# Performance work log

Hardware: AMD Instinct MI355X
Metric: run time of the kernel (lower is better)

The kernel has to match this reference:

```python
import jax, jax.numpy as jnp
import numpy as np

RADIUS = 1.0
N_NORM = 1  # default n_norm in the torch module


def setup_inputs() -> dict:
    key = jax.random.key(0)
    k1, k2, k3 = jax.random.split(key, 3)
    batch, n, c_in, c_out = 8, 2048, 64, 64
    features = jax.random.normal(k1, (batch, n, c_in), dtype=jnp.float32)
    geometry = jax.random.normal(k2, (batch, n, 3), dtype=jnp.float32)
    # learned per-edge kernel weight: K(diff)[o,i] = sum_x diff[x] * Wk[x,o,i]
    Wk = jax.random.normal(k3, (3, c_out, c_in), dtype=jnp.float32) * 0.1
    return {"features": features, "geometry": geometry, "Wk": Wk}


def reference(features, geometry, Wk):
    # diff[z,a,b,:] = geometry[z,b] - geometry[z,a]   (rb - ra in the torch code)
    diff = geometry[:, None, :, :] - geometry[:, :, None, :]  # [z, a, b, 3]
    norm = jnp.sqrt(jnp.sum(diff * diff, axis=-1))            # [z, a, b]
    # Dense masked formulation: padding every point's neighbor list to k = n
    # with rel_mask zeros is mathematically identical to the torch variable-k
    # padding (masked entries contribute nothing to the einsum reduce).
    rel_mask = (norm < RADIUS).astype(features.dtype)         # [z, a, b]
    # Fused reduce. Original: einsum('zab,zabij,zabj->zai', mask, K(diff), feat[nei])
    # with K(diff)[z,a,b,i,j] = einsum('zabx,xij->zabij', diff, Wk). We contract
    # over b first to avoid materializing the [z,a,b,i,j] kernel tensor.
    s = jnp.einsum('zab,zabx,zbj->zaxj', rel_mask, diff, features)  # [z, a, 3, c_in]
    out = jnp.einsum('zaxj,xij->zai', s, Wk) / jnp.sqrt(jnp.asarray(N_NORM, features.dtype))
    return out
```

## Files before the change

### kernel.cpp

```cpp
#include <hip/hip_runtime.h>
#include <stdint.h>

#define NPTS 2048

#define BP_OFF    0ULL
#define BP_BYTES  (8ULL * 16 * 64 * 1024)
#define W2F_OFF   (BP_OFF + BP_BYTES)
#define W2F_BYTES (24ULL * 1024)
#define WXF_OFF   (W2F_OFF + W2F_BYTES)
#define WXF_BYTES (24ULL * 1024)
#define MW_OFF    (WXF_OFF + WXF_BYTES)
#define MW_BYTES  (8ULL * 32 * 64 * 256)

typedef __attribute__((ext_vector_type(8))) short bf16x8;
typedef __attribute__((ext_vector_type(4))) float f32x4;
typedef __attribute__((ext_vector_type(4))) unsigned int u32x4;

__device__ __forceinline__ unsigned f2bf(float f) {
  union { float f; unsigned u; } v; v.f = f;
  return (v.u + 0x7FFFu + ((v.u >> 16) & 1u)) >> 16;
}

__device__ __forceinline__ bf16x8 unpack_mask(unsigned mq) {
  const unsigned dep0 = ((mq & 15u) * 0x204081u) & 0x01010101u;
  const unsigned dep1 = (((mq >> 4) & 15u) * 0x204081u) & 0x01010101u;
  u32x4 aw;
  aw[0] = __builtin_amdgcn_perm(dep0, 0u, 0x0C050C04u) * 0x3F80u;
  aw[1] = __builtin_amdgcn_perm(dep0, 0u, 0x0C070C06u) * 0x3F80u;
  aw[2] = __builtin_amdgcn_perm(dep1, 0u, 0x0C050C04u) * 0x3F80u;
  aw[3] = __builtin_amdgcn_perm(dep1, 0u, 0x0C070C06u) * 0x3F80u;
  union { u32x4 u; bf16x8 h; } cv; cv.u = aw;
  return cv.h;
}

__global__ __launch_bounds__(256, 2) void k1_prep(const float* __restrict__ feat,
                                                  const float* __restrict__ geom,
                                                  const float* __restrict__ Wk,
                                                  unsigned char* __restrict__ ws) {
  const int blk = blockIdx.x, t = threadIdx.x;
  if (blk < 512) {
    const int z = blk >> 6, s = blk & 63;
    __shared__ float FT[64][37];
    __shared__ float g[96];
    __shared__ float gxp[2048], gyp[2048], gzp[2048];
    const float* fz = feat + ((size_t)z * NPTS + s * 32) * 64;
    const float* gz = geom + (size_t)z * NPTS * 3;
    {
      const int row = t >> 3, j0 = (t & 7) << 3;
      const float4 v0 = *(const float4*)&fz[row * 64 + j0];
      const float4 v1 = *(const float4*)&fz[row * 64 + j0 + 4];
      FT[j0 + 0][row] = v0.x; FT[j0 + 1][row] = v0.y;
      FT[j0 + 2][row] = v0.z; FT[j0 + 3][row] = v0.w;
      FT[j0 + 4][row] = v1.x; FT[j0 + 5][row] = v1.y;
      FT[j0 + 6][row] = v1.z; FT[j0 + 7][row] = v1.w;
    }
    if (t < 96) g[t] = gz[s * 96 + t];
    {
      float v[24];
#pragma unroll
      for (int i = 0; i < 6; ++i) *(float4*)&v[i * 4] = *(const float4*)&gz[t * 24 + i * 4];
#pragma unroll
      for (int i = 0; i < 8; ++i) {
        const int pp = i * 256 + t;
        gxp[pp] = v[i * 3 + 0]; gyp[pp] = v[i * 3 + 1]; gzp[pp] = v[i * 3 + 2];
      }
    }
    __syncthreads();

    {
      const int w = t >> 6, L = t & 63;
      const int nn = L >> 2, k0 = (L & 3) * 8;
      const int j = w * 16 + nn;
      float f[8];
#pragma unroll
      for (int i = 0; i < 8; ++i) f[i] = FT[j][k0 + i];
      float gx[3][8];
#pragma unroll
      for (int x = 0; x < 3; ++x)
#pragma unroll
        for (int i = 0; i < 8; ++i) gx[x][i] = g[(k0 + i) * 3 + x];
      unsigned char* base = ws + BP_OFF + (size_t)z * 1048576 + (size_t)w * 65536 +
                            (size_t)s * 1024 + L * 16;
#pragma unroll
      for (int it = 0; it < 4; ++it) {
        u32x4 pv;
#pragma unroll
        for (int p = 0; p < 4; ++p) {
          float f0 = f[2 * p], f1 = f[2 * p + 1];
          if (it < 3) { f0 *= gx[it][2 * p]; f1 *= gx[it][2 * p + 1]; }
          pv[p] = f2bf(f0) | (f2bf(f1) << 16);
        }
        *(u32x4*)(base + (size_t)it * 4 * 65536) = pv;
      }
    }

    {
      float ax[8], ay[8], az[8];
#pragma unroll
      for (int i = 0; i < 8; ++i) {
        const int pp = i * 256 + t;
        ax[i] = gxp[pp]; ay[i] = gyp[pp]; az[i] = gzp[pp];
      }
      unsigned bits[8] = {0, 0, 0, 0, 0, 0, 0, 0};
      for (int j = 0; j < 32; ++j) {
        const float bx = g[j * 3 + 0], by = g[j * 3 + 1], bz = g[j * 3 + 2];
#pragma unroll
        for (int i = 0; i < 8; ++i) {
          const float d0 = bx - ax[i], d1 = by - ay[i], d2 = bz - az[i];
          const float n2 = fmaf(d2, d2, fmaf(d1, d1, d0 * d0));
          bits[i] |= (n2 < 1.0f ? 1u : 0u) << j;
        }
      }
      unsigned int* mw = (unsigned int*)(ws + MW_OFF);
#pragma unroll
      for (int i = 0; i < 8; ++i) {
        const int r = t * 8 + i;
        mw[(((size_t)z * 32 + (r >> 6)) * 64 + s) * 64 + (r & 15) * 4 + ((r >> 4) & 3)] = bits[i];
      }
    }
  } else if (blk == 512) {
    for (int e = t; e < 1536; e += 256) {
      const int frag = e >> 6, lp = e & 63, nn = lp >> 2, qd = lp & 3;
      const int kb = frag >> 2, cb = frag & 3;
      u32x4 pv;
#pragma unroll
      for (int p = 0; p < 4; ++p) {
        const int k0 = kb * 32 + qd * 8 + 2 * p;
        const float v0 = Wk[(k0 >> 6) * 4096 + (cb * 16 + nn) * 64 + (k0 & 63)];
        const float v1 = Wk[((k0 + 1) >> 6) * 4096 + (cb * 16 + nn) * 64 + ((k0 + 1) & 63)];
        pv[p] = f2bf(v0) | (f2bf(v1) << 16);
      }
      *(u32x4*)(ws + W2F_OFF + (size_t)frag * 1024 + lp * 16) = pv;
    }
  } else {
    for (int e = t; e < 1536; e += 256) {
      const int frag = e >> 6, lp = e & 63, nn = lp >> 2, qd = lp & 3;
      const int kb = frag / 12, cb = frag % 12, xi = cb * 16 + nn;
      u32x4 pv;
#pragma unroll
      for (int p = 0; p < 4; ++p) {
        const int k0 = kb * 32 + qd * 8 + 2 * p;
        const float v0 = Wk[(xi >> 6) * 4096 + (xi & 63) * 64 + k0];
        const float v1 = Wk[(xi >> 6) * 4096 + (xi & 63) * 64 + k0 + 1];
        pv[p] = f2bf(v0) | (f2bf(v1) << 16);
      }
      *(u32x4*)(ws + WXF_OFF + (size_t)frag * 1024 + lp * 16) = pv;
    }
  }
}

__global__ __launch_bounds__(256, 2) void k2_gemm(const float* __restrict__ geom,
                                                  const unsigned char* __restrict__ ws,
                                                  float* __restrict__ out) {
  __shared__ __align__(16) unsigned short Ct[64 * 128];

  const int t = threadIdx.x, lane = t & 63, w = t >> 6;
  const int quad = (lane >> 4) & 3, n = lane & 15;
  const int bx = blockIdx.x;
  const int z = bx & 7, at = (bx >> 3) & 31, ch = bx >> 8;
  const int a0 = at * 64;
  const int fragoff = n * 64 + quad * 16;
  const int qsh = quad * 8;

  const unsigned char* bpz = ws + BP_OFF + (size_t)z * 1048576 +
                             (size_t)(ch * 8 + 2 * w) * 65536;
  const unsigned char* mwz = ws + MW_OFF + ((size_t)z * 32 + at) * 16384;

  f32x4 acc[4][2];
#pragma unroll
  for (int rg = 0; rg < 4; ++rg)
#pragma unroll
    for (int cb = 0; cb < 2; ++cb)
#pragma unroll
      for (int r = 0; r < 4; ++r) acc[rg][cb][r] = 0.f;

  bf16x8 Bf[2][2];
  u32x4 Mf[2];
#pragma unroll
  for (int sl = 0; sl < 2; ++sl) {
#pragma unroll
    for (int cb = 0; cb < 2; ++cb)
      Bf[sl][cb] = *(const bf16x8*)(bpz + (size_t)cb * 65536 + (size_t)sl * 1024 + fragoff);
    Mf[sl] = *(const u32x4*)(mwz + sl * 256 + n * 16);
  }

#define KSTEP(S, SL)                                                           \
  {                                                                            \
    const u32x4 mw = Mf[SL];                                                   \
    _Pragma("unroll") for (int rg = 0; rg < 4; ++rg) {                         \
      const bf16x8 Af = unpack_mask((mw[rg] >> qsh) & 0xFFu);                  \
      _Pragma("unroll") for (int cb = 0; cb < 2; ++cb)                         \
        acc[rg][cb] = __builtin_amdgcn_mfma_f32_16x16x32_bf16(                 \
            Af, Bf[SL][cb], acc[rg][cb], 0, 0, 0);                             \
    }                                                                          \
    const int sp = (S) + 2 > 63 ? 63 : (S) + 2;                                \
    Mf[SL] = *(const u32x4*)(mwz + sp * 256 + n * 16);                         \
    _Pragma("unroll") for (int cb = 0; cb < 2; ++cb)                           \
      Bf[SL][cb] = *(const bf16x8*)(bpz + (size_t)cb * 65536 +                 \
                                    (size_t)sp * 1024 + fragoff);              \
  }

  for (int s2 = 0; s2 < 64; s2 += 2) {
    KSTEP(s2, 0)
    KSTEP(s2 + 1, 1)
  }
#undef KSTEP

#pragma unroll
  for (int rg = 0; rg < 4; ++rg)
#pragma unroll
    for (int cb = 0; cb < 2; ++cb)
#pragma unroll
      for (int r = 0; r < 4; ++r) {
        const int row = rg * 16 + quad * 4 + r;
        const int col = w * 32 + cb * 16 + n;
        Ct[row * 128 + ((((col >> 3) ^ (row & 15)) & 15) << 3) + (col & 7)] =
            (unsigned short)f2bf(acc[rg][cb][r]);
      }
  __syncthreads();

  const int lm = 16 * w + n;
  bf16x8 Across[4];
#pragma unroll
  for (int kbl = 0; kbl < 4; ++kbl) {
    const int chunk = ((kbl * 4 + quad) ^ (lm & 15)) & 15;
    Across[kbl] = *(const bf16x8*)&Ct[lm * 128 + (chunk << 3)];
  }

  const unsigned char* w2f = ws + W2F_OFF;
  const unsigned char* wxf = ws + WXF_OFF;

  if (ch == 0) {
    f32x4 mn[4];
#pragma unroll
    for (int i = 0; i < 4; ++i)
#pragma unroll
      for (int r = 0; r < 4; ++r) mn[i][r] = 0.f;
#pragma unroll
    for (int kbl = 0; kbl < 4; ++kbl)
#pragma unroll
      for (int cb = 0; cb < 4; ++cb) {
        const bf16x8 Bfr = *(const bf16x8*)(w2f + (size_t)(kbl * 4 + cb) * 1024 + fragoff);
        mn[cb] = __builtin_amdgcn_mfma_f32_16x16x32_bf16(Across[kbl], Bfr, mn[cb], 0, 0, 0);
      }
#pragma unroll
    for (int r = 0; r < 4; ++r) {
      const int af = a0 + 16 * w + quad * 4 + r;
#pragma unroll
      for (int cb = 0; cb < 4; ++cb)
        atomicAdd(&out[((size_t)z * NPTS + af) * 64 + cb * 16 + n], mn[cb][r]);
    }
  } else {
    f32x4 mn[4], V[12];
#pragma unroll
    for (int i = 0; i < 4; ++i)
#pragma unroll
      for (int r = 0; r < 4; ++r) mn[i][r] = 0.f;
#pragma unroll
    for (int i = 0; i < 12; ++i)
#pragma unroll
      for (int r = 0; r < 4; ++r) V[i][r] = 0.f;
#pragma unroll
    for (int kbl = 0; kbl < 2; ++kbl)
#pragma unroll
      for (int cb = 0; cb < 4; ++cb) {
        const bf16x8 Bfr = *(const bf16x8*)(w2f + (size_t)((4 + kbl) * 4 + cb) * 1024 + fragoff);
        mn[cb] = __builtin_amdgcn_mfma_f32_16x16x32_bf16(Across[kbl], Bfr, mn[cb], 0, 0, 0);
      }
#pragma unroll
    for (int kbl = 0; kbl < 2; ++kbl)
#pragma unroll
      for (int cb = 0; cb < 12; ++cb) {
        const bf16x8 Bfr = *(const bf16x8*)(wxf + (size_t)(kbl * 12 + cb) * 1024 + fragoff);
        V[cb] = __builtin_amdgcn_mfma_f32_16x16x32_bf16(Across[2 + kbl], Bfr, V[cb], 0, 0, 0);
      }
#pragma unroll
    for (int r = 0; r < 4; ++r) {
      const int af = a0 + 16 * w + quad * 4 + r;
      const float g0 = geom[((size_t)z * NPTS + af) * 3 + 0];
      const float g1 = geom[((size_t)z * NPTS + af) * 3 + 1];
      const float g2 = geom[((size_t)z * NPTS + af) * 3 + 2];
#pragma unroll
      for (int cb = 0; cb < 4; ++cb) {
        const float v = mn[cb][r] - g0 * V[cb][r] - g1 * V[cb + 4][r] - g2 * V[cb + 8][r];
        atomicAdd(&out[((size_t)z * NPTS + af) * 64 + cb * 16 + n], v);
      }
    }
  }
}

extern "C" void kernel_launch(void* const* d_in, const int* in_sizes, int n_in,
                              void* d_out, int out_size, void* d_ws, size_t ws_size,
                              hipStream_t stream) {
  const float* feat = (const float*)d_in[0];
  const float* geom = (const float*)d_in[1];
  const float* Wk   = (const float*)d_in[2];
  float* out = (float*)d_out;
  unsigned char* ws = (unsigned char*)d_ws;

  hipMemsetAsync(out, 0, (size_t)out_size * sizeof(float), stream);
  k1_prep<<<dim3(514), 256, 0, stream>>>(feat, geom, Wk, ws);
  k2_gemm<<<dim3(512), 256, 0, stream>>>(geom, ws, out);
}
```

Measured before the change: 108.6 us.

## Merge K-split blocks into 512-thread blocks, drop atomics and memset

Each 64-point tile, previously split across two 256-thread blocks by channel half, is now handled by one 512-thread block whose eight waves cover all 256 columns. Partial results are staged in fp32 shared memory, and four waves run the full second-stage GEMM with plain stores. This removes the output memset and the atomicAdd traffic, and the prefetch depth in the main loop grows from 2 to 4 steps. In exchange the grid is halved to 256 blocks, which may leave CUs idle, register pressure rises from the deeper prefetch, and the epilogue uses only half the waves.

```diff
diff --git a/kernel.cpp b/kernel.cpp
--- a/kernel.cpp
+++ b/kernel.cpp
@@ -19,6 +19,15 @@
 __device__ __forceinline__ unsigned f2bf(float f) {
   union { float f; unsigned u; } v; v.f = f;
   return (v.u + 0x7FFFu + ((v.u >> 16) & 1u)) >> 16;
+}
+
+__device__ __forceinline__ bf16x8 pack8(const float4 a, const float4 b) {
+  u32x4 r;
+  r[0] = f2bf(a.x) | (f2bf(a.y) << 16);
+  r[1] = f2bf(a.z) | (f2bf(a.w) << 16);
+  r[2] = f2bf(b.x) | (f2bf(b.y) << 16);
+  r[3] = f2bf(b.z) | (f2bf(b.w) << 16);
+  union { u32x4 u; bf16x8 h; } c; c.u = r; return c.h;
 }
 
 __device__ __forceinline__ bf16x8 unpack_mask(unsigned mq) {
@@ -149,21 +158,19 @@
   }
 }
 
-__global__ __launch_bounds__(256, 2) void k2_gemm(const float* __restrict__ geom,
+__global__ __launch_bounds__(512, 2) void k2_gemm(const float* __restrict__ geom,
                                                   const unsigned char* __restrict__ ws,
                                                   float* __restrict__ out) {
-  __shared__ __align__(16) unsigned short Ct[64 * 128];
+  __shared__ __align__(16) float Ct[64 * 256];
 
   const int t = threadIdx.x, lane = t & 63, w = t >> 6;
   const int quad = (lane >> 4) & 3, n = lane & 15;
   const int bx = blockIdx.x;
-  const int z = bx & 7, at = (bx >> 3) & 31, ch = bx >> 8;
-  const int a0 = at * 64;
+  const int z = bx & 7, at = bx >> 3, a0 = at * 64;
   const int fragoff = n * 64 + quad * 16;
   const int qsh = quad * 8;
 
-  const unsigned char* bpz = ws + BP_OFF + (size_t)z * 1048576 +
-                             (size_t)(ch * 8 + 2 * w) * 65536;
+  const unsigned char* bpz = ws + BP_OFF + (size_t)z * 1048576 + (size_t)(2 * w) * 65536;
   const unsigned char* mwz = ws + MW_OFF + ((size_t)z * 32 + at) * 16384;
 
   f32x4 acc[4][2];
@@ -174,10 +181,10 @@
 #pragma unroll
       for (int r = 0; r < 4; ++r) acc[rg][cb][r] = 0.f;
 
-  bf16x8 Bf[2][2];
-  u32x4 Mf[2];
-#pragma unroll
-  for (int sl = 0; sl < 2; ++sl) {
+  bf16x8 Bf[4][2];
+  u32x4 Mf[4];
+#pragma unroll
+  for (int sl = 0; sl < 4; ++sl) {
 #pragma unroll
     for (int cb = 0; cb < 2; ++cb)
       Bf[sl][cb] = *(const bf16x8*)(bpz + (size_t)cb * 65536 + (size_t)sl * 1024 + fragoff);
@@ -193,16 +200,15 @@
         acc[rg][cb] = __builtin_amdgcn_mfma_f32_16x16x32_bf16(                 \
             Af, Bf[SL][cb], acc[rg][cb], 0, 0, 0);                             \
     }                                                                          \
-    const int sp = (S) + 2 > 63 ? 63 : (S) + 2;                                \
+    const int sp = (S) + 4 > 63 ? 63 : (S) + 4;                                \
     Mf[SL] = *(const u32x4*)(mwz + sp * 256 + n * 16);                         \
     _Pragma("unroll") for (int cb = 0; cb < 2; ++cb)                           \
       Bf[SL][cb] = *(const bf16x8*)(bpz + (size_t)cb * 65536 +                 \
                                     (size_t)sp * 1024 + fragoff);              \
   }
 
-  for (int s2 = 0; s2 < 64; s2 += 2) {
-    KSTEP(s2, 0)
-    KSTEP(s2 + 1, 1)
+  for (int s4 = 0; s4 < 64; s4 += 4) {
+    KSTEP(s4 + 0, 0) KSTEP(s4 + 1, 1) KSTEP(s4 + 2, 2) KSTEP(s4 + 3, 3)
   }
 #undef KSTEP
 
@@ -213,67 +219,50 @@
 #pragma unroll
       for (int r = 0; r < 4; ++r) {
         const int row = rg * 16 + quad * 4 + r;
-        const int col = w * 32 + cb * 16 + n;
-        Ct[row * 128 + ((((col >> 3) ^ (row & 15)) & 15) << 3) + (col & 7)] =
-            (unsigned short)f2bf(acc[rg][cb][r]);
+        const int col = 32 * w + cb * 16 + n;
+        Ct[row * 256 + (((col >> 2) ^ row) << 2) + (col & 3)] = acc[rg][cb][r];
       }
   __syncthreads();
 
-  const int lm = 16 * w + n;
-  bf16x8 Across[4];
-#pragma unroll
-  for (int kbl = 0; kbl < 4; ++kbl) {
-    const int chunk = ((kbl * 4 + quad) ^ (lm & 15)) & 15;
-    Across[kbl] = *(const bf16x8*)&Ct[lm * 128 + (chunk << 3)];
-  }
-
-  const unsigned char* w2f = ws + W2F_OFF;
-  const unsigned char* wxf = ws + WXF_OFF;
-
-  if (ch == 0) {
-    f32x4 mn[4];
+  if (w < 4) {
+    const int lm = 16 * w + n;
+    bf16x8 Across[8];
+#pragma unroll
+    for (int kb = 0; kb < 8; ++kb) {
+      const int c0 = (kb * 8 + quad * 2) ^ lm;
+      const int c1 = (kb * 8 + quad * 2 + 1) ^ lm;
+      const float4 f0 = *(const float4*)&Ct[lm * 256 + c0 * 4];
+      const float4 f1 = *(const float4*)&Ct[lm * 256 + c1 * 4];
+      Across[kb] = pack8(f0, f1);
+    }
+
+    f32x4 mn[4], V[12];
 #pragma unroll
     for (int i = 0; i < 4; ++i)
 #pragma unroll
       for (int r = 0; r < 4; ++r) mn[i][r] = 0.f;
 #pragma unroll
-    for (int kbl = 0; kbl < 4; ++kbl)
+    for (int i = 0; i < 12; ++i)
+#pragma unroll
+      for (int r = 0; r < 4; ++r) V[i][r] = 0.f;
+
+    const unsigned char* w2f = ws + W2F_OFF;
+    const unsigned char* wxf = ws + WXF_OFF;
+#pragma unroll
+    for (int kb = 0; kb < 6; ++kb)
 #pragma unroll
       for (int cb = 0; cb < 4; ++cb) {
-        const bf16x8 Bfr = *(const bf16x8*)(w2f + (size_t)(kbl * 4 + cb) * 1024 + fragoff);
-        mn[cb] = __builtin_amdgcn_mfma_f32_16x16x32_bf16(Across[kbl], Bfr, mn[cb], 0, 0, 0);
-      }
-#pragma unroll
-    for (int r = 0; r < 4; ++r) {
-      const int af = a0 + 16 * w + quad * 4 + r;
-#pragma unroll
-      for (int cb = 0; cb < 4; ++cb)
-        atomicAdd(&out[((size_t)z * NPTS + af) * 64 + cb * 16 + n], mn[cb][r]);
-    }
-  } else {
-    f32x4 mn[4], V[12];
-#pragma unroll
-    for (int i = 0; i < 4; ++i)
-#pragma unroll
-      for (int r = 0; r < 4; ++r) mn[i][r] = 0.f;
-#pragma unroll
-    for (int i = 0; i < 12; ++i)
-#pragma unroll
-      for (int r = 0; r < 4; ++r) V[i][r] = 0.f;
-#pragma unroll
-    for (int kbl = 0; kbl < 2; ++kbl)
-#pragma unroll
-      for (int cb = 0; cb < 4; ++cb) {
-        const bf16x8 Bfr = *(const bf16x8*)(w2f + (size_t)((4 + kbl) * 4 + cb) * 1024 + fragoff);
-        mn[cb] = __builtin_amdgcn_mfma_f32_16x16x32_bf16(Across[kbl], Bfr, mn[cb], 0, 0, 0);
-      }
-#pragma unroll
-    for (int kbl = 0; kbl < 2; ++kbl)
+        const bf16x8 Bfr = *(const bf16x8*)(w2f + (size_t)(kb * 4 + cb) * 1024 + fragoff);
+        mn[cb] = __builtin_amdgcn_mfma_f32_16x16x32_bf16(Across[kb], Bfr, mn[cb], 0, 0, 0);
+      }
+#pragma unroll
+    for (int kb = 0; kb < 2; ++kb)
 #pragma unroll
       for (int cb = 0; cb < 12; ++cb) {
-        const bf16x8 Bfr = *(const bf16x8*)(wxf + (size_t)(kbl * 12 + cb) * 1024 + fragoff);
-        V[cb] = __builtin_amdgcn_mfma_f32_16x16x32_bf16(Across[2 + kbl], Bfr, V[cb], 0, 0, 0);
-      }
+        const bf16x8 Bfr = *(const bf16x8*)(wxf + (size_t)(kb * 12 + cb) * 1024 + fragoff);
+        V[cb] = __builtin_amdgcn_mfma_f32_16x16x32_bf16(Across[6 + kb], Bfr, V[cb], 0, 0, 0);
+      }
+
 #pragma unroll
     for (int r = 0; r < 4; ++r) {
       const int af = a0 + 16 * w + quad * 4 + r;
@@ -283,7 +272,7 @@
 #pragma unroll
       for (int cb = 0; cb < 4; ++cb) {
         const float v = mn[cb][r] - g0 * V[cb][r] - g1 * V[cb + 4][r] - g2 * V[cb + 8][r];
-        atomicAdd(&out[((size_t)z * NPTS + af) * 64 + cb * 16 + n], v);
+        out[((size_t)z * NPTS + af) * 64 + cb * 16 + n] = v;
       }
     }
   }
@@ -298,7 +287,6 @@
   float* out = (float*)d_out;
   unsigned char* ws = (unsigned char*)d_ws;
 
-  hipMemsetAsync(out, 0, (size_t)out_size * sizeof(float), stream);
   k1_prep<<<dim3(514), 256, 0, stream>>>(feat, geom, Wk, ws);
-  k2_gemm<<<dim3(512), 256, 0, stream>>>(geom, ws, out);
-}
+  k2_gemm<<<dim3(256), 512, 0, stream>>>(geom, ws, out);
+}
```

Result: faster. 102.9 us (-5.3%).
